# Optimization experiments

Hardware: AMD Instinct MI355X
Metric: run time of the kernel (lower is better)

## Reference

```python
import jax, jax.numpy as jnp
import numpy as np

D = 512       # d_model
H = 8         # n_heads
L = 6         # n_blocks
DFF = 2048    # d_ffn
IN_DIM = 4096
OUT_DIM = 1000
B = 8
S = 512
DK = D // H
EPS = 1e-5
NEG = -1e9    # masked_fill value from source (-1000000000.0)

# sinusoidal positional encoding table (matches Positional_Encoding)
_pos = np.arange(5000)[:, None].astype(np.float64)
_div = np.exp(np.arange(0, D, 2) * (-np.log(10000.0) / D))
_pe = np.zeros((5000, D), np.float32)
_pe[:, 0::2] = np.sin(_pos * _div)
_pe[:, 1::2] = np.cos(_pos * _div)
PE = jnp.asarray(_pe)


def _ln(x, g, b):
    m = jnp.mean(x, -1, keepdims=True)
    v = jnp.var(x, -1, keepdims=True)
    return (x - m) * jax.lax.rsqrt(v + EPS) * g + b


def _attn(q, k, v, causal):
    # q:[B,Sq,D], k/v:[B,Sk,D] -> multi-head attention with source's quirky mask
    b, sq, _ = q.shape
    sk = k.shape[1]
    q = q.reshape(b, sq, H, DK).transpose(0, 2, 1, 3)
    k = k.reshape(b, sk, H, DK).transpose(0, 2, 1, 3)
    v = v.reshape(b, sk, H, DK).transpose(0, 2, 1, 3)
    s = jnp.einsum('bhqd,bhkd->bhqk', q, k) / jnp.sqrt(jnp.asarray(DK, q.dtype))
    mask = s != 0.0  # faithful: source masks positions where score == padding (0)
    if causal:
        mask = mask & jnp.tril(jnp.ones((sq, sk), bool))
    s = jnp.where(mask, s, NEG)
    p = jax.nn.softmax(s, axis=-1)
    o = jnp.einsum('bhqk,bhkd->bhqd', p, v)
    return o.transpose(0, 2, 1, 3).reshape(b, sq, D)


def _ffn(x, w1, b1, w2, b2):
    return jax.nn.relu(x @ w1 + b1) @ w2 + b2


def setup_inputs() -> dict:
    key = jax.random.key(0)
    ks = iter(jax.random.split(key, 40))

    def w(shape, s=0.02):
        return jax.random.normal(next(ks), shape, jnp.float32) * s

    inp = {}
    inp['x'] = jax.random.randint(next(ks), (B, S), 0, IN_DIM)
    inp['target'] = jax.random.randint(next(ks), (B,), 0, OUT_DIM)
    inp['in_emb'] = w((IN_DIM, D), 1.0)
    inp['out_emb'] = w((OUT_DIM, D), 1.0)
    # encoder params (stacked over layers)
    inp['enc_qkv_w'] = w((L, 3, D, D))
    inp['enc_qkv_b'] = w((L, 3, D))
    inp['enc_ln1_g'] = jnp.ones((L, D), jnp.float32)
    inp['enc_ln1_b'] = jnp.zeros((L, D), jnp.float32)
    inp['enc_ffn1_w'] = w((L, D, DFF))
    inp['enc_ffn1_b'] = w((L, DFF))
    inp['enc_ffn2_w'] = w((L, DFF, D))
    inp['enc_ffn2_b'] = w((L, D))
    inp['enc_ln2_g'] = jnp.ones((L, D), jnp.float32)
    inp['enc_ln2_b'] = jnp.zeros((L, D), jnp.float32)
    # decoder params
    inp['dec_qkv1_w'] = w((L, 3, D, D))
    inp['dec_qkv1_b'] = w((L, 3, D))
    inp['dec_ln1_g'] = jnp.ones((L, D), jnp.float32)
    inp['dec_ln1_b'] = jnp.zeros((L, D), jnp.float32)
    inp['dec_qkv2_w'] = w((L, 3, D, D))
    inp['dec_qkv2_b'] = w((L, 3, D))
    inp['dec_ln2_g'] = jnp.ones((L, D), jnp.float32)
    inp['dec_ln2_b'] = jnp.zeros((L, D), jnp.float32)
    inp['dec_ffn1_w'] = w((L, D, DFF))
    inp['dec_ffn1_b'] = w((L, DFF))
    inp['dec_ffn2_w'] = w((L, DFF, D))
    inp['dec_ffn2_b'] = w((L, D))
    inp['dec_ln3_g'] = jnp.ones((L, D), jnp.float32)
    inp['dec_ln3_b'] = jnp.zeros((L, D), jnp.float32)
    inp['out_w'] = w((D, OUT_DIM))
    inp['out_b'] = w((OUT_DIM,))
    return inp


def reference(x, target, in_emb, out_emb,
              enc_qkv_w, enc_qkv_b, enc_ln1_g, enc_ln1_b,
              enc_ffn1_w, enc_ffn1_b, enc_ffn2_w, enc_ffn2_b,
              enc_ln2_g, enc_ln2_b,
              dec_qkv1_w, dec_qkv1_b, dec_ln1_g, dec_ln1_b,
              dec_qkv2_w, dec_qkv2_b, dec_ln2_g, dec_ln2_b,
              dec_ffn1_w, dec_ffn1_b, dec_ffn2_w, dec_ffn2_b,
              dec_ln3_g, dec_ln3_b, out_w, out_b):
    scale = jnp.sqrt(jnp.float32(D))
    # encoder: embed tokens + positional encoding (dropout is identity at eval)
    e = in_emb[x] * scale + PE[None, :S]
    for i in range(L):
        q = e @ enc_qkv_w[i, 0] + enc_qkv_b[i, 0]
        k = e @ enc_qkv_w[i, 1] + enc_qkv_b[i, 1]
        v = e @ enc_qkv_w[i, 2] + enc_qkv_b[i, 2]
        e = _ln(_attn(q, k, v, False) + e, enc_ln1_g[i], enc_ln1_b[i])
        e = _ln(e + _ffn(e, enc_ffn1_w[i], enc_ffn1_b[i], enc_ffn2_w[i], enc_ffn2_b[i]),
                enc_ln2_g[i], enc_ln2_b[i])
    # decoder: target.unsqueeze(1) -> seq len 1
    d = out_emb[target][:, None, :] * scale + PE[None, :1]
    for i in range(L):
        q = d @ dec_qkv1_w[i, 0] + dec_qkv1_b[i, 0]
        k = d @ dec_qkv1_w[i, 1] + dec_qkv1_b[i, 1]
        v = d @ dec_qkv1_w[i, 2] + dec_qkv1_b[i, 2]
        d = _ln(_attn(q, k, v, True) + d, dec_ln1_g[i], dec_ln1_b[i])
        q = d @ dec_qkv2_w[i, 0] + dec_qkv2_b[i, 0]
        k = e @ dec_qkv2_w[i, 1] + dec_qkv2_b[i, 1]
        v = e @ dec_qkv2_w[i, 2] + dec_qkv2_b[i, 2]
        d = _ln(_attn(q, k, v, False) + d, dec_ln2_g[i], dec_ln2_b[i])
        d = _ln(d + _ffn(d, dec_ffn1_w[i], dec_ffn1_b[i], dec_ffn2_w[i], dec_ffn2_b[i]),
                dec_ln3_g[i], dec_ln3_b[i])
    return d @ out_w + out_b  # [B, 1, OUT_DIM] logits (source never applies its softmax)
```

## Files before the change

### kernel.cpp

```cpp
#include <hip/hip_runtime.h>
#include <hip/hip_bf16.h>

#define DM 512
#define NH 8
#define DK 64
#define SEQ 512
#define NB 8
#define NL 6
#define DFF 2048
#define OUTD 1000
#define EMB_SCALE 22.627416997969522f
#define PE_C (-0.017988946039015984f)

typedef __bf16 bf16x8 __attribute__((ext_vector_type(8)));
typedef __bf16 bf16x4 __attribute__((ext_vector_type(4)));
typedef float f32x4 __attribute__((ext_vector_type(4)));

__device__ __forceinline__ void load16_lds(const __bf16* g, __bf16* l) {
  __builtin_amdgcn_global_load_lds(
      (const __attribute__((address_space(1))) void*)g,
      (__attribute__((address_space(3))) void*)l, 16, 0, 0);
}

__device__ __forceinline__ float dot8(bf16x8 w, const float* a) {
  float s = 0.f;
#pragma unroll
  for (int j = 0; j < 8; ++j) s += (float)w[j] * a[j];
  return s;
}

__device__ __forceinline__ void ln_pair(float v0, float v1, int tid,
                                        const float* __restrict__ g,
                                        const float* __restrict__ beta,
                                        float* out, float* ps, float* pq) {
  float s = v0 + v1, sq = v0 * v0 + v1 * v1;
  for (int o = 32; o > 0; o >>= 1) { s += __shfl_xor(s, o); sq += __shfl_xor(sq, o); }
  int wv = tid >> 6;
  if ((tid & 63) == 0) { ps[wv] = s; pq[wv] = sq; }
  __syncthreads();
  s = ps[0] + ps[1] + ps[2] + ps[3];
  sq = pq[0] + pq[1] + pq[2] + pq[3];
  float mean = s * (1.f / DM);
  float rstd = rsqrtf(sq * (1.f / DM) - mean * mean + 1e-5f);
  out[tid] = (v0 - mean) * rstd * g[tid] + beta[tid];
  out[tid + 256] = (v1 - mean) * rstd * g[tid + 256] + beta[tid + 256];
  __syncthreads();
}

__global__ __launch_bounds__(256) void pe_kernel(float* __restrict__ pe) {
  int s = blockIdx.x;
  int d2 = threadIdx.x;
  float div = expf((float)(2 * d2) * PE_C);
  float arg = (float)s * div;
  pe[(size_t)s * DM + 2 * d2] = sinf(arg);
  pe[(size_t)s * DM + 2 * d2 + 1] = cosf(arg);
}

__global__ __launch_bounds__(256) void embed_enc(const int* __restrict__ x,
                                                 const float* __restrict__ emb,
                                                 const float* __restrict__ pe,
                                                 float* __restrict__ e,
                                                 __bf16* __restrict__ eb) {
  int idx = blockIdx.x * 256 + threadIdx.x;
  int d2 = idx & 255;
  int bs = idx >> 8;
  int s = bs & (SEQ - 1);
  int tok = x[bs];
  float2 ev = ((const float2*)(emb + (size_t)tok * DM))[d2];
  float2 pv = ((const float2*)(pe + (size_t)s * DM))[d2];
  float v0 = ev.x * EMB_SCALE + pv.x;
  float v1 = ev.y * EMB_SCALE + pv.y;
  ((float2*)e)[idx] = make_float2(v0, v1);
  union { __bf16 h[2]; unsigned u; } pk;
  pk.h[0] = (__bf16)v0; pk.h[1] = (__bf16)v1;
  ((unsigned*)eb)[idx] = pk.u;
}

__global__ __launch_bounds__(256) void transpose_w3(
    const float* __restrict__ W0, __bf16* __restrict__ T0, int n0,
    const float* __restrict__ W1, __bf16* __restrict__ T1, int n1,
    const float* __restrict__ W2, __bf16* __restrict__ T2,
    long zmul2, long zadd2, int K, int N) {
  __shared__ float t[32][33];
  int z = blockIdx.z;
  const float* W;
  __bf16* WT;
  if (z < n0) {
    W = W0 + (size_t)z * K * N; WT = T0 + (size_t)z * K * N;
  } else if (z < n0 + n1) {
    int zz = z - n0;
    W = W1 + (size_t)zz * K * N; WT = T1 + (size_t)zz * K * N;
  } else {
    int zz = z - n0 - n1;
    W = W2 + (size_t)(zz * zmul2 + zadd2) * K * N;
    WT = T2 + (size_t)zz * K * N;
  }
  int k0 = blockIdx.y * 32, n0b = blockIdx.x * 32;
  int tx = threadIdx.x & 7, ty = threadIdx.x >> 3;
  float4 v = *(const float4*)&W[(size_t)(k0 + ty) * N + n0b + tx * 4];
  t[ty][tx * 4 + 0] = v.x; t[ty][tx * 4 + 1] = v.y;
  t[ty][tx * 4 + 2] = v.z; t[ty][tx * 4 + 3] = v.w;
  __syncthreads();
  bf16x4 o;
  o[0] = (__bf16)t[tx * 4 + 0][ty];
  o[1] = (__bf16)t[tx * 4 + 1][ty];
  o[2] = (__bf16)t[tx * 4 + 2][ty];
  o[3] = (__bf16)t[tx * 4 + 3][ty];
  *(bf16x4*)&WT[(size_t)(n0b + ty) * K + k0 + tx * 4] = o;
}

__global__ __launch_bounds__(256) void transpose_ow(const float* __restrict__ W,
                                                    __bf16* __restrict__ WT) {
  __shared__ float t[32][33];
  int n0 = blockIdx.x * 32, k0 = blockIdx.y * 32;
  int tid = threadIdx.x;
  for (int i = tid; i < 1024; i += 256) {
    int kk = i >> 5, nn = i & 31;
    t[kk][nn] = (n0 + nn < OUTD) ? W[(size_t)(k0 + kk) * OUTD + n0 + nn] : 0.f;
  }
  __syncthreads();
  for (int i = tid; i < 1024; i += 256) {
    int nn = i >> 5, kk = i & 31;
    if (n0 + nn < OUTD)
      WT[(size_t)(n0 + nn) * DM + k0 + kk] = (__bf16)t[kk][nn];
  }
}

template <int BN, int SK, bool RELU, bool WF32, bool WBF16, bool TRV, bool KVM>
__global__ __launch_bounds__(256) void mfma_gemm(
    const __bf16* __restrict__ A, const __bf16* __restrict__ BT,
    const float* __restrict__ bias, float* __restrict__ C,
    __bf16* __restrict__ Cb, __bf16* __restrict__ Vt, int M, int N, int K,
    long btStride, long bStride, long cStride) {
  int gx = gridDim.x, gy = gridDim.y;
  int lin = blockIdx.x + gx * (blockIdx.y + gy * blockIdx.z);
  int xcd = lin & 7, li = lin >> 3;
  int yc = gy >> 3;
  int bx = li % gx;
  int t2 = li / gx;
  int by = xcd * yc + (t2 % yc);
  int z = t2 / yc;

  if (SK == 1) {
    if (KVM) {
      long idx = (long)(z >> 1) * 3 + 1 + (z & 1);
      BT += idx * btStride;
      bias += idx * bStride;
    } else {
      BT += (size_t)z * btStride;
      bias += (size_t)z * bStride;
    }
  }
  if (WF32) C += (size_t)z * cStride;
  if (WBF16) Cb += (size_t)z * cStride;

  constexpr int NI = BN / 32;
  __shared__ __bf16 As[2][128 * 64];
  __shared__ __bf16 Bs[2][BN * 64];

  int tid = threadIdx.x;
  int wave = tid >> 6, lane = tid & 63;
  int wm = wave >> 1, wn = wave & 1;
  int quad = lane >> 4, l16 = lane & 15;
  int rlane = lane >> 3, c8 = lane & 7;
  int m0 = by * 128, n0 = bx * BN;
  int gcol = ((c8 ^ rlane) * 8);

  f32x4 acc[4][NI];
#pragma unroll
  for (int i = 0; i < 4; ++i)
#pragma unroll
    for (int j = 0; j < NI; ++j) acc[i][j] = (f32x4){0.f, 0.f, 0.f, 0.f};

  auto stage = [&](int buf, int k0) {
#pragma unroll
    for (int j = 0; j < 4; ++j) {
      int rb = j * 32 + wave * 8;
      load16_lds(&A[(size_t)(m0 + rb + rlane) * K + k0 + gcol],
                 &As[buf][rb * 64]);
    }
#pragma unroll
    for (int j = 0; j < BN / 32; ++j) {
      int rb = j * 32 + wave * 8;
      load16_lds(&BT[(size_t)(n0 + rb + rlane) * K + k0 + gcol],
                 &Bs[buf][rb * 64]);
    }
  };

  int kLen = (SK > 1) ? (K / SK) : K;
  int kBeg = (SK > 1) ? z * kLen : 0;
  const int NT = kLen >> 6;
  stage(0, kBeg);
  __syncthreads();
  for (int t = 0; t < NT; ++t) {
    int cur = t & 1;
    if (t + 1 < NT) stage(cur ^ 1, kBeg + ((t + 1) << 6));
#pragma unroll
    for (int kk = 0; kk < 64; kk += 32) {
      bf16x8 af[4], bfr[NI];
#pragma unroll
      for (int i = 0; i < 4; ++i) {
        int row = wm * 64 + i * 16 + l16;
        af[i] = *(const bf16x8*)&As[cur][row * 64 + ((((kk >> 3) + quad) ^ (row & 7)) * 8)];
      }
#pragma unroll
      for (int i = 0; i < NI; ++i) {
        int row = wn * (BN / 2) + i * 16 + l16;
        bfr[i] = *(const bf16x8*)&Bs[cur][row * 64 + ((((kk >> 3) + quad) ^ (row & 7)) * 8)];
      }
#pragma unroll
      for (int mi = 0; mi < 4; ++mi)
#pragma unroll
        for (int ni = 0; ni < NI; ++ni)
          acc[mi][ni] = __builtin_amdgcn_mfma_f32_16x16x32_bf16(
              af[mi], bfr[ni], acc[mi][ni], 0, 0, 0);
    }
    __syncthreads();
  }

#pragma unroll
  for (int ni = 0; ni < NI; ++ni) {
    int col = n0 + wn * (BN / 2) + ni * 16 + l16;
    float bv = (SK == 1 || z == 0) ? bias[col] : 0.f;
    if (TRV && z == 2) {
      int b = m0 >> 9;
#pragma unroll
      for (int mi = 0; mi < 4; ++mi) {
        int srow = (m0 & 511) + wm * 64 + mi * 16 + quad * 4;
        bf16x4 pk;
#pragma unroll
        for (int r = 0; r < 4; ++r) pk[r] = (__bf16)(acc[mi][ni][r] + bv);
        *(bf16x4*)&Vt[((size_t)(b * 512 + col)) * 512 + srow] = pk;
      }
    } else {
#pragma unroll
      for (int mi = 0; mi < 4; ++mi) {
#pragma unroll
        for (int r = 0; r < 4; ++r) {
          int row = m0 + wm * 64 + mi * 16 + quad * 4 + r;
          float v = acc[mi][ni][r] + bv;
          if (RELU) v = fmaxf(v, 0.f);
          if (WF32) C[(size_t)row * N + col] = v;
          if (WBF16) Cb[(size_t)row * N + col] = (__bf16)v;
        }
      }
    }
  }
}

#define SCP 520
__global__ __launch_bounds__(256) void attn_mfma(const __bf16* __restrict__ QKV,
                                                 const __bf16* __restrict__ Vt,
                                                 float* __restrict__ O) {
  __shared__ __bf16 Sc[16 * SCP];
  __shared__ __bf16 Tt[2][64 * 64];

  const long ACTL = (long)NB * SEQ * DM;
  int tid = threadIdx.x;
  int wave = tid >> 6, lane = tid & 63;
  int quad = lane >> 4, l16 = lane & 15;
  int rlane = lane >> 3, c8 = lane & 7;
  int lin = blockIdx.x + gridDim.x * blockIdx.y;
  int xcd = lin & 7, li = lin >> 3;
  int yc = gridDim.y >> 3;
  int q0 = (li % gridDim.x) * 16;
  int bh = xcd * yc + li / gridDim.x;
  int b = bh >> 3, h = bh & 7;
  const __bf16* Q = QKV;
  const __bf16* Kp = QKV + ACTL;
  size_t baseQ = ((size_t)b * SEQ + q0) * DM + h * DK;
  size_t baseK = ((size_t)b * SEQ) * DM + h * DK;
  const __bf16* VtB = Vt + ((size_t)(b * 512 + h * 64)) * 512;
  int gcol = (c8 ^ rlane) * 8;

  bf16x8 af0 = *(const bf16x8*)&Q[baseQ + (size_t)l16 * DM + quad * 8];
  bf16x8 af1 = *(const bf16x8*)&Q[baseQ + (size_t)l16 * DM + 32 + quad * 8];

  auto stageK = [&](int buf, int kt) {
#pragma unroll
    for (int j = 0; j < 2; ++j) {
      int row = j * 32 + wave * 8 + rlane;
      load16_lds(&Kp[baseK + (size_t)(kt * 64 + row) * DM + gcol],
                 &Tt[buf][(j * 32 + wave * 8) * 64]);
    }
  };
  auto stageV = [&](int buf, int kt) {
#pragma unroll
    for (int j = 0; j < 2; ++j) {
      int row = j * 32 + wave * 8 + rlane;
      load16_lds(&VtB[(size_t)row * 512 + kt * 64 + gcol],
                 &Tt[buf][(j * 32 + wave * 8) * 64]);
    }
  };

  stageK(0, 0);
  __syncthreads();
  for (int kt = 0; kt < 8; ++kt) {
    int cur = kt & 1;
    if (kt < 7) stageK(cur ^ 1, kt + 1);
    f32x4 acc = (f32x4){0.f, 0.f, 0.f, 0.f};
    int krow = wave * 16 + l16, sw = krow & 7;
    bf16x8 b0 = *(const bf16x8*)&Tt[cur][krow * 64 + ((quad ^ sw) * 8)];
    bf16x8 b1 = *(const bf16x8*)&Tt[cur][krow * 64 + (((4 + quad) ^ sw) * 8)];
    acc = __builtin_amdgcn_mfma_f32_16x16x32_bf16(af0, b0, acc, 0, 0, 0);
    acc = __builtin_amdgcn_mfma_f32_16x16x32_bf16(af1, b1, acc, 0, 0, 0);
#pragma unroll
    for (int r = 0; r < 4; ++r)
      Sc[(quad * 4 + r) * SCP + kt * 64 + wave * 16 + l16] =
          (__bf16)(acc[r] * 0.125f);
    __syncthreads();
  }

  stageV(0, 0);

#pragma unroll
  for (int rr = 0; rr < 4; ++rr) {
    int r = wave * 4 + rr;
    float v[8];
    float mx = -1e30f;
#pragma unroll
    for (int j = 0; j < 8; ++j) {
      v[j] = (float)Sc[r * SCP + j * 64 + lane];
      mx = fmaxf(mx, v[j]);
    }
    for (int o = 32; o > 0; o >>= 1) mx = fmaxf(mx, __shfl_xor(mx, o));
    float sum = 0.f;
#pragma unroll
    for (int j = 0; j < 8; ++j) { v[j] = __expf(v[j] - mx); sum += v[j]; }
    for (int o = 32; o > 0; o >>= 1) sum += __shfl_xor(sum, o);
    float inv = 1.f / sum;
#pragma unroll
    for (int j = 0; j < 8; ++j)
      Sc[r * SCP + j * 64 + lane] = (__bf16)(v[j] * inv);
  }
  __syncthreads();

  f32x4 oacc = (f32x4){0.f, 0.f, 0.f, 0.f};
  for (int kt = 0; kt < 8; ++kt) {
    int cur = kt & 1;
    if (kt < 7) stageV(cur ^ 1, kt + 1);
    int drow = wave * 16 + l16, sw = drow & 7;
#pragma unroll
    for (int kk = 0; kk < 64; kk += 32) {
      bf16x8 pa = *(const bf16x8*)&Sc[l16 * SCP + kt * 64 + kk + quad * 8];
      bf16x8 vb = *(const bf16x8*)&Tt[cur][drow * 64 + ((((kk >> 3) + quad) ^ sw) * 8)];
      oacc = __builtin_amdgcn_mfma_f32_16x16x32_bf16(pa, vb, oacc, 0, 0, 0);
    }
    __syncthreads();
  }
#pragma unroll
  for (int r = 0; r < 4; ++r)
    O[((size_t)b * SEQ + q0 + quad * 4 + r) * DM + h * DK + wave * 16 + l16] =
        oacc[r];
}

template <bool WB>
__global__ __launch_bounds__(256) void add_ln(
    const float* __restrict__ x, const float* __restrict__ x2,
    const float* __restrict__ res, const float* __restrict__ cbias,
    const float* __restrict__ g, const float* __restrict__ beta,
    float* __restrict__ y, __bf16* __restrict__ yb) {
  int row = blockIdx.x;
  int tid = threadIdx.x;
  float2 xv = ((const float2*)(x + (size_t)row * DM))[tid];
  float2 rv = ((const float2*)(res + (size_t)row * DM))[tid];
  float v0 = xv.x + rv.x;
  float v1 = xv.y + rv.y;
  if (cbias) {
    float2 cb = ((const float2*)cbias)[tid];
    v0 += cb.x; v1 += cb.y;
  }
  if (x2) {
    float2 x2v = ((const float2*)(x2 + (size_t)row * DM))[tid];
    v0 += x2v.x; v1 += x2v.y;
  }
  float s = v0 + v1, sq = v0 * v0 + v1 * v1;
  for (int o = 32; o > 0; o >>= 1) {
    s += __shfl_xor(s, o);
    sq += __shfl_xor(sq, o);
  }
  __shared__ float ps[4], pq[4];
  int wv = tid >> 6;
  if ((tid & 63) == 0) { ps[wv] = s; pq[wv] = sq; }
  __syncthreads();
  s = ps[0] + ps[1] + ps[2] + ps[3];
  sq = pq[0] + pq[1] + pq[2] + pq[3];
  float mean = s * (1.f / DM);
  float var = sq * (1.f / DM) - mean * mean;
  float rstd = rsqrtf(var + 1e-5f);
  float2 gg = ((const float2*)g)[tid];
  float2 bb = ((const float2*)beta)[tid];
  float o0 = (v0 - mean) * rstd * gg.x + bb.x;
  float o1 = (v1 - mean) * rstd * gg.y + bb.y;
  ((float2*)(y + (size_t)row * DM))[tid] = make_float2(o0, o1);
  if (WB) {
    union { __bf16 h[2]; unsigned u; } pk;
    pk.h[0] = (__bf16)o0; pk.h[1] = (__bf16)o1;
    ((unsigned*)(yb + (size_t)row * DM))[tid] = pk.u;
  }
}


template <bool FIRST>
__global__ __launch_bounds__(256) void dec_attn(
    const float* __restrict__ dfp, const float* __restrict__ xp,
    const float* __restrict__ g3, const float* __restrict__ b3,
    const int* __restrict__ target, const float* __restrict__ emb,
    const __bf16* __restrict__ WvT, const float* __restrict__ bv,
    const float* __restrict__ g1, const float* __restrict__ b1ln,
    const __bf16* __restrict__ WqT, const float* __restrict__ qb,
    const __bf16* __restrict__ Kb, const __bf16* __restrict__ Vb,
    float* __restrict__ da, float* __restrict__ tbuf) {
  __shared__ float arow[DM];
  __shared__ float trow[DM];
  __shared__ float red[4][64];
  __shared__ float q[64];
  __shared__ float sc[SEQ];
  __shared__ float wred[4];
  __shared__ float ps[4], pq[4];

  int bh = blockIdx.x, b = bh >> 3, h = bh & 7;
  int tid = threadIdx.x, lane = tid & 63, wave = tid >> 6;

  if (FIRST) {
    int tok = target[b];
    arow[tid] = emb[(size_t)tok * DM + tid] * EMB_SCALE + ((tid & 1) ? 1.f : 0.f);
    arow[tid + 256] =
        emb[(size_t)tok * DM + tid + 256] * EMB_SCALE + ((tid & 1) ? 1.f : 0.f);
    __syncthreads();
  } else {
    float v0 = dfp[(size_t)b * DM + tid] + xp[(size_t)b * DM + tid];
    float v1 = dfp[(size_t)b * DM + tid + 256] + xp[(size_t)b * DM + tid + 256];
    ln_pair(v0, v1, tid, g3, b3, arow, ps, pq);
  }

  float o0, o1;
  {
    const __bf16* w = &WvT[(size_t)tid * DM];
    float acc = 0.f;
#pragma unroll 4
    for (int k = 0; k < DM; k += 8) acc += dot8(*(const bf16x8*)&w[k], &arow[k]);
    o0 = arow[tid] + acc + bv[tid];
  }
  {
    const __bf16* w = &WvT[(size_t)(tid + 256) * DM];
    float acc = 0.f;
#pragma unroll 4
    for (int k = 0; k < DM; k += 8) acc += dot8(*(const bf16x8*)&w[k], &arow[k]);
    o1 = arow[tid + 256] + acc + bv[tid + 256];
  }
  ln_pair(o0, o1, tid, g1, b1ln, trow, ps, pq);
  if (h == 0) {
    tbuf[(size_t)b * DM + tid] = trow[tid];
    tbuf[(size_t)b * DM + tid + 256] = trow[tid + 256];
  }

  {
    int c = tid & 63, s = tid >> 6;
    const __bf16* w = &WqT[(size_t)(h * 64 + c) * DM + s * 128];
    float acc = 0.f;
#pragma unroll
    for (int k = 0; k < 128; k += 8)
      acc += dot8(*(const bf16x8*)&w[k], &trow[s * 128 + k]);
    red[s][c] = acc;
  }
  __syncthreads();
  if (tid < 64)
    q[tid] = red[0][tid] + red[1][tid] + red[2][tid] + red[3][tid] + qb[h * 64 + tid];
  __syncthreads();

  for (int key = tid; key < SEQ; key += 256) {
    const __bf16* kp = &Kb[((size_t)b * SEQ + key) * DM + h * 64];
    float acc = 0.f;
#pragma unroll
    for (int k = 0; k < 64; k += 8) acc += dot8(*(const bf16x8*)&kp[k], &q[k]);
    sc[key] = acc * 0.125f;
  }
  __syncthreads();
  float m = -1e30f;
  for (int j = tid; j < SEQ; j += 256) m = fmaxf(m, sc[j]);
  for (int o = 32; o > 0; o >>= 1) m = fmaxf(m, __shfl_xor(m, o));
  if (lane == 0) wred[wave] = m;
  __syncthreads();
  m = fmaxf(fmaxf(wred[0], wred[1]), fmaxf(wred[2], wred[3]));
  float sum = 0.f;
  for (int j = tid; j < SEQ; j += 256) {
    float p = __expf(sc[j] - m);
    sc[j] = p;
    sum += p;
  }
  for (int o = 32; o > 0; o >>= 1) sum += __shfl_xor(sum, o);
  __syncthreads();
  if (lane == 0) wred[wave] = sum;
  __syncthreads();
  float inv = 1.f / (wred[0] + wred[1] + wred[2] + wred[3]);

  {
    int d = tid & 63, s = tid >> 6;
    float acc = 0.f;
    const __bf16* vp = &Vb[((size_t)b * SEQ + s * 128) * DM + h * 64 + d];
#pragma unroll 8
    for (int k = 0; k < 128; ++k) acc += sc[s * 128 + k] * (float)vp[(size_t)k * DM];
    red[s][d] = acc;
  }
  __syncthreads();
  if (tid < 64)
    da[(size_t)b * DM + h * 64 + tid] =
        (red[0][tid] + red[1][tid] + red[2][tid] + red[3][tid]) * inv;
}

__global__ __launch_bounds__(256) void dec_ffn1f(
    const float* __restrict__ da, const float* __restrict__ tbuf,
    const float* __restrict__ g2, const float* __restrict__ b2ln,
    const __bf16* __restrict__ W1T, const float* __restrict__ b1,
    float* __restrict__ h, float* __restrict__ xbuf) {
  __shared__ float a[8][DM];
  __shared__ float ps[4], pq[4];
  int tid = threadIdx.x, lane = tid & 63, wave = tid >> 6;
  for (int r = 0; r < 8; ++r) {
    float v0 = da[(size_t)r * DM + tid] + tbuf[(size_t)r * DM + tid];
    float v1 = da[(size_t)r * DM + tid + 256] + tbuf[(size_t)r * DM + tid + 256];
    ln_pair(v0, v1, tid, g2, b2ln, a[r], ps, pq);
  }
  int col = blockIdx.x * 4 + wave;
  bf16x8 w = *(const bf16x8*)&W1T[(size_t)col * DM + lane * 8];
  float acc[8];
#pragma unroll
  for (int r = 0; r < 8; ++r) acc[r] = dot8(w, &a[r][lane * 8]);
#pragma unroll
  for (int r = 0; r < 8; ++r)
    for (int o = 32; o > 0; o >>= 1) acc[r] += __shfl_xor(acc[r], o);
  if (lane == 0) {
    float bb = b1[col];
#pragma unroll
    for (int r = 0; r < 8; ++r) h[(size_t)r * DFF + col] = fmaxf(acc[r] + bb, 0.f);
  }
  if (blockIdx.x == 0) {
#pragma unroll
    for (int r = 0; r < 8; ++r) {
      xbuf[(size_t)r * DM + tid] = a[r][tid];
      xbuf[(size_t)r * DM + tid + 256] = a[r][tid + 256];
    }
  }
}

__global__ __launch_bounds__(256) void dec_ffn2(
    const float* __restrict__ h, const __bf16* __restrict__ W2T,
    const float* __restrict__ b2, float* __restrict__ df) {
  __shared__ float red[4][8];
  int tid = threadIdx.x, lane = tid & 63, wave = tid >> 6;
  int c = wave >> 1, half = wave & 1;
  int col = blockIdx.x * 2 + c;
  int k0 = half * 1024 + lane * 8;
  bf16x8 w0 = *(const bf16x8*)&W2T[(size_t)col * DFF + k0];
  bf16x8 w1 = *(const bf16x8*)&W2T[(size_t)col * DFF + k0 + 512];
  float acc[8];
#pragma unroll
  for (int r = 0; r < 8; ++r) {
    float4 h0a = *(const float4*)&h[(size_t)r * DFF + k0];
    float4 h0b = *(const float4*)&h[(size_t)r * DFF + k0 + 4];
    float4 h1a = *(const float4*)&h[(size_t)r * DFF + k0 + 512];
    float4 h1b = *(const float4*)&h[(size_t)r * DFF + k0 + 516];
    float hh0[8] = {h0a.x, h0a.y, h0a.z, h0a.w, h0b.x, h0b.y, h0b.z, h0b.w};
    float hh1[8] = {h1a.x, h1a.y, h1a.z, h1a.w, h1b.x, h1b.y, h1b.z, h1b.w};
    acc[r] = dot8(w0, hh0) + dot8(w1, hh1);
  }
#pragma unroll
  for (int r = 0; r < 8; ++r)
    for (int o = 32; o > 0; o >>= 1) acc[r] += __shfl_xor(acc[r], o);
  if (lane == 0) {
#pragma unroll
    for (int r = 0; r < 8; ++r) red[wave][r] = acc[r];
  }
  __syncthreads();
  if (tid < 16) {
    int cc = tid >> 3, r = tid & 7;
    int ocol = blockIdx.x * 2 + cc;
    df[(size_t)r * DM + ocol] =
        red[cc * 2][r] + red[cc * 2 + 1][r] + b2[ocol];
  }
}

__global__ __launch_bounds__(256) void dec_outf(
    const float* __restrict__ df, const float* __restrict__ xbuf,
    const float* __restrict__ g3, const float* __restrict__ b3,
    const __bf16* __restrict__ WoT, const float* __restrict__ ob,
    float* __restrict__ out) {
  __shared__ float a[8][DM];
  __shared__ float ps[4], pq[4];
  int tid = threadIdx.x, lane = tid & 63, wave = tid >> 6;
  for (int r = 0; r < 8; ++r) {
    float v0 = df[(size_t)r * DM + tid] + xbuf[(size_t)r * DM + tid];
    float v1 = df[(size_t)r * DM + tid + 256] + xbuf[(size_t)r * DM + tid + 256];
    ln_pair(v0, v1, tid, g3, b3, a[r], ps, pq);
  }
  int col = blockIdx.x * 4 + wave;
  bf16x8 w = *(const bf16x8*)&WoT[(size_t)col * DM + lane * 8];
  float acc[8];
#pragma unroll
  for (int r = 0; r < 8; ++r) acc[r] = dot8(w, &a[r][lane * 8]);
#pragma unroll
  for (int r = 0; r < 8; ++r)
    for (int o = 32; o > 0; o >>= 1) acc[r] += __shfl_xor(acc[r], o);
  if (lane == 0) {
    float bb = ob[col];
#pragma unroll
    for (int r = 0; r < 8; ++r) out[(size_t)r * OUTD + col] = acc[r] + bb;
  }
}

extern "C" void kernel_launch(void* const* d_in, const int* in_sizes, int n_in,
                              void* d_out, int out_size, void* d_ws, size_t ws_size,
                              hipStream_t stream) {
  const int* x = (const int*)d_in[0];
  const int* target = (const int*)d_in[1];
  const float* in_emb = (const float*)d_in[2];
  const float* out_emb = (const float*)d_in[3];
  const float* enc_qkv_w = (const float*)d_in[4];
  const float* enc_qkv_b = (const float*)d_in[5];
  const float* enc_ln1_g = (const float*)d_in[6];
  const float* enc_ln1_b = (const float*)d_in[7];
  const float* enc_ffn1_w = (const float*)d_in[8];
  const float* enc_ffn1_b = (const float*)d_in[9];
  const float* enc_ffn2_w = (const float*)d_in[10];
  const float* enc_ffn2_b = (const float*)d_in[11];
  const float* enc_ln2_g = (const float*)d_in[12];
  const float* enc_ln2_b = (const float*)d_in[13];
  const float* dec_qkv1_w = (const float*)d_in[14];
  const float* dec_qkv1_b = (const float*)d_in[15];
  const float* dec_ln1_g = (const float*)d_in[16];
  const float* dec_ln1_b = (const float*)d_in[17];
  const float* dec_qkv2_w = (const float*)d_in[18];
  const float* dec_qkv2_b = (const float*)d_in[19];
  const float* dec_ln2_g = (const float*)d_in[20];
  const float* dec_ln2_b = (const float*)d_in[21];
  const float* dec_ffn1_w = (const float*)d_in[22];
  const float* dec_ffn1_b = (const float*)d_in[23];
  const float* dec_ffn2_w = (const float*)d_in[24];
  const float* dec_ffn2_b = (const float*)d_in[25];
  const float* dec_ln3_g = (const float*)d_in[26];
  const float* dec_ln3_b = (const float*)d_in[27];
  const float* out_w = (const float*)d_in[28];
  const float* out_b = (const float*)d_in[29];

  const long ACTL = (long)NB * SEQ * DM;
  const int M = NB * SEQ;
  const long WQS = (long)DM * DM;
  const long WFS = (long)DM * DFF;

  char* p = (char*)d_ws;
  float* e = (float*)p;            p += ACTL * 4;
  float* tb = (float*)p;           p += ACTL * 4;
  float* pe = (float*)p;           p += (long)SEQ * DM * 4;
  float* dd = (float*)p;           p += NB * DM * 4;
  float* da = (float*)p;           p += NB * DM * 4;
  float* dh = (float*)p;           p += NB * DFF * 4;
  float* df = (float*)p;           p += NB * DM * 4;
  p = (char*)(((uintptr_t)p + 255) & ~(uintptr_t)255);
  __bf16* eb = (__bf16*)p;         p += ACTL * 2;
  __bf16* qkvb = (__bf16*)p;       p += 3 * ACTL * 2;
  __bf16* hbb = (__bf16*)p;        p += (long)M * DFF * 2;
  __bf16* kvb = (__bf16*)p;        p += 12L * ACTL * 2;
  __bf16* wtq = (__bf16*)p;        p += 18L * WQS * 2;
  __bf16* wtf1 = (__bf16*)p;       p += 6L * WFS * 2;
  __bf16* wtf2 = (__bf16*)p;       p += 6L * WFS * 2;
  __bf16* wtd = (__bf16*)p;        p += 18L * WQS * 2;
  __bf16* wtd1 = (__bf16*)p;       p += 18L * WQS * 2;
  __bf16* wf1t = (__bf16*)p;       p += 6L * WFS * 2;
  __bf16* wf2t = (__bf16*)p;       p += 6L * WFS * 2;
  __bf16* wot = (__bf16*)p;        p += (long)OUTD * DM * 2;

  __bf16* vtb = qkvb + 2 * ACTL;
  float* tb2 = (float*)kvb;
  float* tbuf = dd;
  float* xbuf = pe;

  pe_kernel<<<SEQ, 256, 0, stream>>>(pe);
  transpose_w3<<<dim3(16, 16, 42), 256, 0, stream>>>(
      enc_qkv_w, wtq, 18, dec_qkv2_w, wtd, 18, dec_qkv1_w, wtd1, 3, 2, DM, DM);
  transpose_w3<<<dim3(64, 16, 12), 256, 0, stream>>>(
      enc_ffn1_w, wtf1, 6, dec_ffn1_w, wf1t, 6, nullptr, nullptr, 0, 0, DM, DFF);
  transpose_w3<<<dim3(16, 64, 12), 256, 0, stream>>>(
      enc_ffn2_w, wtf2, 6, dec_ffn2_w, wf2t, 6, nullptr, nullptr, 0, 0, DFF, DM);
  transpose_ow<<<dim3(32, 16), 256, 0, stream>>>(out_w, wot);

  embed_enc<<<(M * DM / 2) / 256, 256, 0, stream>>>(x, in_emb, pe, e, eb);
  for (int i = 0; i < NL; ++i) {
    mfma_gemm<64, 1, false, false, true, true, false><<<dim3(8, 32, 3), 256, 0, stream>>>(
        eb, wtq + (size_t)i * 3 * WQS, enc_qkv_b + (size_t)i * 3 * DM,
        nullptr, qkvb, vtb, M, DM, DM, WQS, DM, ACTL);
    attn_mfma<<<dim3(SEQ / 16, NB * NH), 256, 0, stream>>>(qkvb, vtb, tb);
    add_ln<true><<<M, 256, 0, stream>>>(tb, nullptr, e, nullptr,
                                        enc_ln1_g + i * DM, enc_ln1_b + i * DM,
                                        e, eb);
    mfma_gemm<64, 1, true, false, true, false, false><<<dim3(32, 32, 1), 256, 0, stream>>>(
        eb, wtf1 + (size_t)i * WFS, enc_ffn1_b + (size_t)i * DFF,
        nullptr, hbb, nullptr, M, DFF, DM, 0, 0, 0);
    mfma_gemm<64, 2, false, true, false, false, false><<<dim3(8, 32, 2), 256, 0, stream>>>(
        hbb, wtf2 + (size_t)i * WFS, enc_ffn2_b + (size_t)i * DM,
        tb, nullptr, nullptr, M, DM, DFF, 0, 0, (long)(tb2 - tb));
    add_ln<true><<<M, 256, 0, stream>>>(tb, tb2, e, nullptr,
                                        enc_ln2_g + i * DM, enc_ln2_b + i * DM,
                                        e, eb);
  }

  mfma_gemm<64, 1, false, false, true, false, true><<<dim3(8, 32, 12), 256, 0, stream>>>(
      eb, wtd, dec_qkv2_b, nullptr, kvb, nullptr, M, DM, DM, WQS, DM, ACTL);

  for (int i = 0; i < NL; ++i) {
    const __bf16* Wv = wtd1 + (size_t)i * WQS;
    const float* bvp = dec_qkv1_b + ((size_t)i * 3 + 2) * DM;
    const __bf16* Wq = wtd + (size_t)i * 3 * WQS;
    const float* qbp = dec_qkv2_b + (size_t)i * 3 * DM;
    const __bf16* Kb = kvb + (size_t)i * 2 * ACTL;
    const __bf16* Vb = kvb + ((size_t)i * 2 + 1) * ACTL;
    if (i == 0)
      dec_attn<true><<<64, 256, 0, stream>>>(
          nullptr, nullptr, nullptr, nullptr, target, out_emb,
          Wv, bvp, dec_ln1_g + i * DM, dec_ln1_b + i * DM,
          Wq, qbp, Kb, Vb, da, tbuf);
    else
      dec_attn<false><<<64, 256, 0, stream>>>(
          df, xbuf, dec_ln3_g + (i - 1) * DM, dec_ln3_b + (i - 1) * DM,
          nullptr, nullptr,
          Wv, bvp, dec_ln1_g + i * DM, dec_ln1_b + i * DM,
          Wq, qbp, Kb, Vb, da, tbuf);
    dec_ffn1f<<<DFF / 4, 256, 0, stream>>>(
        da, tbuf, dec_ln2_g + i * DM, dec_ln2_b + i * DM,
        wf1t + (size_t)i * WFS, dec_ffn1_b + (size_t)i * DFF, dh, xbuf);
    dec_ffn2<<<DM / 2, 256, 0, stream>>>(
        dh, wf2t + (size_t)i * WFS, dec_ffn2_b + (size_t)i * DM, df);
  }

  dec_outf<<<OUTD / 4, 256, 0, stream>>>(df, xbuf, dec_ln3_g + 5 * DM,
                                         dec_ln3_b + 5 * DM, wot, out_b,
                                         (float*)d_out);
}
```

Baseline: 1.114 ms.

## Read GEMM A operand and attention K/V directly from global memory

The GEMM kernel stops staging A tiles in LDS and instead has each wave read its A fragments straight from global memory. B is staged in a single 64x512 LDS chunk per 512-wide K slice rather than double-buffered 64-wide tiles, which removes most of the per-tile barriers. The attention kernel likewise drops LDS staging of K and V^T and loads MFMA operands directly from global, which removes the per-iteration __syncthreads. This trades LDS traffic and synchronisation for uncoalesced, latency-exposed global loads that rely on the cache, and the B chunk occupies 64KB of LDS, which may reduce occupancy.

Measured after the change: 1.555 ms. 1.4x slower.

```diff
diff --git a/kernel.cpp b/kernel.cpp
--- a/kernel.cpp
+++ b/kernel.cpp
@@ -132,6 +132,7 @@
     const float* __restrict__ bias, float* __restrict__ C,
     __bf16* __restrict__ Cb, __bf16* __restrict__ Vt, int M, int N, int K,
     long btStride, long bStride, long cStride) {
+  static_assert(BN == 64, "structure assumes BN=64");
   int gx = gridDim.x, gy = gridDim.y;
   int lin = blockIdx.x + gx * (blockIdx.y + gy * blockIdx.z);
   int xcd = lin & 7, li = lin >> 3;
@@ -154,73 +155,67 @@
   if (WF32) C += (size_t)z * cStride;
   if (WBF16) Cb += (size_t)z * cStride;
 
-  constexpr int NI = BN / 32;
-  __shared__ __bf16 As[2][128 * 64];
-  __shared__ __bf16 Bs[2][BN * 64];
+  __shared__ __bf16 Bs[64 * 512];
 
   int tid = threadIdx.x;
   int wave = tid >> 6, lane = tid & 63;
   int wm = wave >> 1, wn = wave & 1;
   int quad = lane >> 4, l16 = lane & 15;
-  int rlane = lane >> 3, c8 = lane & 7;
   int m0 = by * 128, n0 = bx * BN;
-  int gcol = ((c8 ^ rlane) * 8);
-
-  f32x4 acc[4][NI];
+
+  f32x4 acc[4][2];
 #pragma unroll
   for (int i = 0; i < 4; ++i)
 #pragma unroll
-    for (int j = 0; j < NI; ++j) acc[i][j] = (f32x4){0.f, 0.f, 0.f, 0.f};
-
-  auto stage = [&](int buf, int k0) {
-#pragma unroll
-    for (int j = 0; j < 4; ++j) {
-      int rb = j * 32 + wave * 8;
-      load16_lds(&A[(size_t)(m0 + rb + rlane) * K + k0 + gcol],
-                 &As[buf][rb * 64]);
-    }
-#pragma unroll
-    for (int j = 0; j < BN / 32; ++j) {
-      int rb = j * 32 + wave * 8;
-      load16_lds(&BT[(size_t)(n0 + rb + rlane) * K + k0 + gcol],
-                 &Bs[buf][rb * 64]);
-    }
-  };
+    for (int j = 0; j < 2; ++j) acc[i][j] = (f32x4){0.f, 0.f, 0.f, 0.f};
 
   int kLen = (SK > 1) ? (K / SK) : K;
   int kBeg = (SK > 1) ? z * kLen : 0;
-  const int NT = kLen >> 6;
-  stage(0, kBeg);
-  __syncthreads();
-  for (int t = 0; t < NT; ++t) {
-    int cur = t & 1;
-    if (t + 1 < NT) stage(cur ^ 1, kBeg + ((t + 1) << 6));
-#pragma unroll
-    for (int kk = 0; kk < 64; kk += 32) {
-      bf16x8 af[4], bfr[NI];
-#pragma unroll
-      for (int i = 0; i < 4; ++i) {
-        int row = wm * 64 + i * 16 + l16;
-        af[i] = *(const bf16x8*)&As[cur][row * 64 + ((((kk >> 3) + quad) ^ (row & 7)) * 8)];
-      }
-#pragma unroll
-      for (int i = 0; i < NI; ++i) {
-        int row = wn * (BN / 2) + i * 16 + l16;
-        bfr[i] = *(const bf16x8*)&Bs[cur][row * 64 + ((((kk >> 3) + quad) ^ (row & 7)) * 8)];
-      }
-#pragma unroll
-      for (int mi = 0; mi < 4; ++mi)
-#pragma unroll
-        for (int ni = 0; ni < NI; ++ni)
-          acc[mi][ni] = __builtin_amdgcn_mfma_f32_16x16x32_bf16(
-              af[mi], bfr[ni], acc[mi][ni], 0, 0, 0);
+  const int NC = kLen >> 9;
+
+  const __bf16* arow[4];
+#pragma unroll
+  for (int i = 0; i < 4; ++i)
+    arow[i] = A + (size_t)(m0 + wm * 64 + i * 16 + l16) * K + kBeg;
+
+  for (int c = 0; c < NC; ++c) {
+    if (c) __syncthreads();
+    int kc = kBeg + (c << 9);
+#pragma unroll
+    for (int j = 0; j < 16; ++j) {
+      int row = j * 4 + wave;
+      load16_lds(&BT[(size_t)(n0 + row) * K + kc + ((lane ^ (row & 7)) << 3)],
+                 &Bs[row * 512]);
     }
     __syncthreads();
-  }
-
-#pragma unroll
-  for (int ni = 0; ni < NI; ++ni) {
-    int col = n0 + wn * (BN / 2) + ni * 16 + l16;
+    int cof = c << 9;
+#pragma unroll 2
+    for (int kt = 0; kt < 8; ++kt) {
+#pragma unroll
+      for (int kk = 0; kk < 64; kk += 32) {
+        bf16x8 af[4], bfr[2];
+#pragma unroll
+        for (int i = 0; i < 4; ++i)
+          af[i] = *(const bf16x8*)&arow[i][cof + kt * 64 + kk + quad * 8];
+#pragma unroll
+        for (int i = 0; i < 2; ++i) {
+          int row = wn * 32 + i * 16 + l16;
+          int ck = kt * 8 + (kk >> 3) + quad;
+          bfr[i] = *(const bf16x8*)&Bs[row * 512 + ((ck ^ (row & 7)) << 3)];
+        }
+#pragma unroll
+        for (int mi = 0; mi < 4; ++mi)
+#pragma unroll
+          for (int ni = 0; ni < 2; ++ni)
+            acc[mi][ni] = __builtin_amdgcn_mfma_f32_16x16x32_bf16(
+                af[mi], bfr[ni], acc[mi][ni], 0, 0, 0);
+      }
+    }
+  }
+
+#pragma unroll
+  for (int ni = 0; ni < 2; ++ni) {
+    int col = n0 + wn * 32 + ni * 16 + l16;
     float bv = (SK == 1 || z == 0) ? bias[col] : 0.f;
     if (TRV && z == 2) {
       int b = m0 >> 9;
@@ -253,13 +248,11 @@
                                                  const __bf16* __restrict__ Vt,
                                                  float* __restrict__ O) {
   __shared__ __bf16 Sc[16 * SCP];
-  __shared__ __bf16 Tt[2][64 * 64];
 
   const long ACTL = (long)NB * SEQ * DM;
   int tid = threadIdx.x;
   int wave = tid >> 6, lane = tid & 63;
   int quad = lane >> 4, l16 = lane & 15;
-  int rlane = lane >> 3, c8 = lane & 7;
   int lin = blockIdx.x + gridDim.x * blockIdx.y;
   int xcd = lin & 7, li = lin >> 3;
   int yc = gridDim.y >> 3;
@@ -271,47 +264,25 @@
   size_t baseQ = ((size_t)b * SEQ + q0) * DM + h * DK;
   size_t baseK = ((size_t)b * SEQ) * DM + h * DK;
   const __bf16* VtB = Vt + ((size_t)(b * 512 + h * 64)) * 512;
-  int gcol = (c8 ^ rlane) * 8;
 
   bf16x8 af0 = *(const bf16x8*)&Q[baseQ + (size_t)l16 * DM + quad * 8];
   bf16x8 af1 = *(const bf16x8*)&Q[baseQ + (size_t)l16 * DM + 32 + quad * 8];
 
-  auto stageK = [&](int buf, int kt) {
-#pragma unroll
-    for (int j = 0; j < 2; ++j) {
-      int row = j * 32 + wave * 8 + rlane;
-      load16_lds(&Kp[baseK + (size_t)(kt * 64 + row) * DM + gcol],
-                 &Tt[buf][(j * 32 + wave * 8) * 64]);
-    }
-  };
-  auto stageV = [&](int buf, int kt) {
-#pragma unroll
-    for (int j = 0; j < 2; ++j) {
-      int row = j * 32 + wave * 8 + rlane;
-      load16_lds(&VtB[(size_t)row * 512 + kt * 64 + gcol],
-                 &Tt[buf][(j * 32 + wave * 8) * 64]);
-    }
-  };
-
-  stageK(0, 0);
-  __syncthreads();
+  int krow = wave * 16 + l16;
+#pragma unroll 2
   for (int kt = 0; kt < 8; ++kt) {
-    int cur = kt & 1;
-    if (kt < 7) stageK(cur ^ 1, kt + 1);
+    const __bf16* kp = &Kp[baseK + (size_t)(kt * 64 + krow) * DM];
+    bf16x8 b0 = *(const bf16x8*)&kp[quad * 8];
+    bf16x8 b1 = *(const bf16x8*)&kp[32 + quad * 8];
     f32x4 acc = (f32x4){0.f, 0.f, 0.f, 0.f};
-    int krow = wave * 16 + l16, sw = krow & 7;
-    bf16x8 b0 = *(const bf16x8*)&Tt[cur][krow * 64 + ((quad ^ sw) * 8)];
-    bf16x8 b1 = *(const bf16x8*)&Tt[cur][krow * 64 + (((4 + quad) ^ sw) * 8)];
     acc = __builtin_amdgcn_mfma_f32_16x16x32_bf16(af0, b0, acc, 0, 0, 0);
     acc = __builtin_amdgcn_mfma_f32_16x16x32_bf16(af1, b1, acc, 0, 0, 0);
 #pragma unroll
     for (int r = 0; r < 4; ++r)
       Sc[(quad * 4 + r) * SCP + kt * 64 + wave * 16 + l16] =
           (__bf16)(acc[r] * 0.125f);
-    __syncthreads();
-  }
-
-  stageV(0, 0);
+  }
+  __syncthreads();
 
 #pragma unroll
   for (int rr = 0; rr < 4; ++rr) {
@@ -336,17 +307,15 @@
   __syncthreads();
 
   f32x4 oacc = (f32x4){0.f, 0.f, 0.f, 0.f};
+  int drow = wave * 16 + l16;
+#pragma unroll 2
   for (int kt = 0; kt < 8; ++kt) {
-    int cur = kt & 1;
-    if (kt < 7) stageV(cur ^ 1, kt + 1);
-    int drow = wave * 16 + l16, sw = drow & 7;
 #pragma unroll
     for (int kk = 0; kk < 64; kk += 32) {
       bf16x8 pa = *(const bf16x8*)&Sc[l16 * SCP + kt * 64 + kk + quad * 8];
-      bf16x8 vb = *(const bf16x8*)&Tt[cur][drow * 64 + ((((kk >> 3) + quad) ^ sw) * 8)];
+      bf16x8 vb = *(const bf16x8*)&VtB[(size_t)drow * 512 + kt * 64 + kk + quad * 8];
       oacc = __builtin_amdgcn_mfma_f32_16x16x32_bf16(pa, vb, oacc, 0, 0, 0);
     }
-    __syncthreads();
   }
 #pragma unroll
   for (int r = 0; r < 4; ++r)
```
